# Kernel optimization log

Measured on AMD Instinct MI355X. Metric: run time of the kernel, lower is better.

## Reference

```python
import jax, jax.numpy as jnp
import numpy as np
import math

B, L, H, NH = 4, 2048, 256, 8
DH = H // NH

def setup_inputs() -> dict:
    key = jax.random.key(0)
    ks = jax.random.split(key, 10)
    q = jax.random.normal(ks[0], (B, L, H), dtype=jnp.float32)
    k = jax.random.normal(ks[1], (B, L, H), dtype=jnp.float32)
    v = jax.random.normal(ks[2], (B, L, H), dtype=jnp.float32)
    k_b = jax.random.normal(ks[3], (B, L, H), dtype=jnp.float32)
    mask = jnp.ones((B, L), dtype=jnp.int32)
    # learned params
    scale_w = jax.random.normal(ks[4], (NH, L), dtype=jnp.float32)
    Wb = jax.random.normal(ks[5], (H, H), dtype=jnp.float32) * (1.0 / math.sqrt(H))
    bb = jnp.zeros((H,), dtype=jnp.float32)
    Ww = jax.random.normal(ks[6], (H, H), dtype=jnp.float32) * (1.0 / math.sqrt(H))
    bw = jnp.zeros((H,), dtype=jnp.float32)
    return {"q": q, "k": k, "v": v, "k_b": k_b, "mask": mask,
            "scale_w": scale_w, "Wb": Wb, "bb": bb, "Ww": Ww, "bw": bw}

def _split_heads(x):
    b, l, _ = x.shape
    return x.reshape(b, l, NH, DH).transpose(0, 2, 1, 3)  # [B, NH, L, DH]

def reference(q, k, v, k_b, mask, scale_w, Wb, bb, Ww, bw):
    qh = _split_heads(q)
    kh = _split_heads(k)
    vh = _split_heads(v)
    kb = _split_heads(k_b @ Wb.T + bb)
    # dual QK^T: [B, NH, L, L]
    corr = jnp.einsum('bhqd,bhkd->bhqk', qh, kh) + jnp.einsum('bhqd,bhkd->bhqk', qh, kb)
    corr = corr * (1.0 / math.sqrt(DH))
    # per-head, per-query-position learned scale
    corr = corr * scale_w[None, :, :, None]
    # mask over key positions: [B,1,1,L]
    corr = jnp.where(mask[:, None, None, :] == 0, jnp.float32(-1e9), corr)
    prob = jax.nn.softmax(corr, axis=-1)
    hidden = jnp.einsum('bhqk,bhkd->bhqd', prob, vh)  # [B, NH, L, DH]
    hidden = hidden.transpose(0, 2, 1, 3).reshape(hidden.shape[0], -1, NH * DH)
    return hidden @ Ww.T + bw
```

## Files before the change

kernel.cpp:

```cpp
#include <hip/hip_runtime.h>
#include <stdint.h>
#include <stddef.h>


#define B_ 4
#define L_ 2048
#define H_ 256
#define NH_ 8
#define DH_ 32

typedef float    f32x4  __attribute__((ext_vector_type(4)));
typedef float    f32x16 __attribute__((ext_vector_type(16)));
typedef __bf16   bf16x8 __attribute__((ext_vector_type(8)));
typedef uint16_t u16x4  __attribute__((ext_vector_type(4)));
typedef uint16_t u16x8  __attribute__((ext_vector_type(8)));

static __device__ __forceinline__ uint16_t f2bf(float f) {
  __bf16 h = (__bf16)f;
  return __builtin_bit_cast(uint16_t, h);
}

static __device__ __forceinline__ void gl16(const void* g, void* l) {
  __builtin_amdgcn_global_load_lds(
      (const __attribute__((address_space(1))) uint32_t*)g,
      (__attribute__((address_space(3))) uint32_t*)l, 16, 0, 0);
}

#define OFF_KSUM 0
#define OFF_VTP  (OFF_KSUM + (size_t)B_*NH_*L_*DH_*2)
#define OFF_HID  (OFF_VTP  + (size_t)B_*NH_*L_*DH_*2)
#define OFF_FLAG (OFF_HID  + (size_t)B_*L_*H_*2)


__global__ __launch_bounds__(512, 1) void prep_k(const float* __restrict__ kb,
                                                 const float* __restrict__ wb,
                                                 const float* __restrict__ kin,
                                                 const float* __restrict__ bb,
                                                 const float* __restrict__ v,
                                                 const int* __restrict__ mask,
                                                 uint16_t* __restrict__ ksum_out,
                                                 uint16_t* __restrict__ vtp,
                                                 int* __restrict__ maskflag) {
  __shared__ uint16_t SM[65536];
  const int tid = threadIdx.x;

  if (blockIdx.x == 768) {
    if (tid < 4) maskflag[tid] = 0;
    __syncthreads();
    int b = tid >> 7, seg = tid & 127;
    int bad = 0;
#pragma unroll
    for (int i = 0; i < 16; i++) bad |= (mask[b * 2048 + seg * 16 + i] == 0);
    if (bad) atomicOr(&maskflag[b], 1);
    return;
  }

  if (blockIdx.x < 512) {
    uint16_t (*T)[33] = (uint16_t(*)[33])SM;
    const int bh = blockIdx.x >> 4, t = blockIdx.x & 15;
    const int b = bh >> 3, h = bh & 7;
    {
      int r = tid >> 2, qtr = tid & 3;
      const float* src = v + ((size_t)(b * 2048 + t * 128 + r)) * 256 + h * 32 + qtr * 8;
      f32x4 s0 = *(const f32x4*)(src);
      f32x4 s1 = *(const f32x4*)(src + 4);
#pragma unroll
      for (int i = 0; i < 4; i++) {
        T[r][qtr * 8 + i]     = f2bf(s0[i]);
        T[r][qtr * 8 + 4 + i] = f2bf(s1[i]);
      }
    }
    __syncthreads();
    {
      int slot = tid >> 5, d = tid & 31;
      int kg = slot >> 2, s = (slot >> 1) & 1, hii = slot & 1;
      u16x8 val;
#pragma unroll
      for (int e = 0; e < 8; e++) {
        int key = kg * 32 + s * 16 + 4 * hii + (e & 3) + 8 * (e >> 2);
        val[e] = T[key][d];
      }
      *(u16x8*)(vtp + (size_t)bh * 65536 + t * 4096 + slot * 256 + d * 8) = val;
    }
    return;
  }

  uint16_t* WB = SM;
  const int mblk = blockIdx.x - 512;
  const int wv = tid >> 6, lane = tid & 63;
  const int g = lane >> 4, qi = lane & 15;
  const int rt = wv & 1, ch = wv >> 1;
  const int m = mblk * 32 + rt * 16 + qi;
  const int n0 = ch * 64;

#pragma unroll
  for (int s = 0; s < 16; s++) {
    int gid = s * 512 + tid;
    int n = gid >> 5, gl = gid & 31;
    const float* src = wb + (size_t)n * 256 + gl * 8;
    f32x4 a0 = *(const f32x4*)src;
    f32x4 a1 = *(const f32x4*)(src + 4);
    u16x8 val;
#pragma unroll
    for (int i = 0; i < 4; i++) { val[i] = f2bf(a0[i]); val[4 + i] = f2bf(a1[i]); }
    *(u16x8*)&WB[n * 256 + (gl ^ (n & 7)) * 8] = val;
  }
  __syncthreads();

  f32x4 acc[4];
#pragma unroll
  for (int i = 0; i < 4; i++) acc[i] = (f32x4){0.f, 0.f, 0.f, 0.f};

#pragma unroll
  for (int ks = 0; ks < 8; ks++) {
    const float* ap = kb + (size_t)m * 256 + ks * 32 + g * 8;
    f32x4 a0 = *(const f32x4*)ap;
    f32x4 a1 = *(const f32x4*)(ap + 4);
    bf16x8 af;
#pragma unroll
    for (int i = 0; i < 4; i++) { af[i] = (__bf16)a0[i]; af[4 + i] = (__bf16)a1[i]; }
#pragma unroll
    for (int nt = 0; nt < 4; nt++) {
      int n = n0 + nt * 16 + qi;
      bf16x8 bf = *(const bf16x8*)&WB[n * 256 + ((ks * 4 + g) ^ (n & 7)) * 8];
      acc[nt] = __builtin_amdgcn_mfma_f32_16x16x32_bf16(af, bf, acc[nt], 0, 0, 0);
    }
  }
#pragma unroll
  for (int nt = 0; nt < 4; nt++) {
    int n = n0 + nt * 16 + qi;
    float bbv = bb[n];
    int h = n >> 5, d = n & 31;
#pragma unroll
    for (int j = 0; j < 4; j++) {
      int mr = mblk * 32 + rt * 16 + g * 4 + j;
      float val = acc[nt][j] + bbv + kin[(size_t)mr * 256 + n];
      int bq = mr >> 11, l = mr & 2047;
      size_t off = (size_t)(bq * 8 + h) * 65536 +
                   (l >> 5) * 1024 + (d >> 4) * 512 + (l & 31) * 16 + (d & 15);
      ksum_out[off] = f2bf(val);
    }
  }
}

__global__ __launch_bounds__(256, 2) void attn_k(const float* __restrict__ q,
                                                 const int* __restrict__ mask,
                                                 const float* __restrict__ scale_w,
                                                 const uint16_t* __restrict__ ksum,
                                                 const uint16_t* __restrict__ vtp,
                                                 const int* __restrict__ maskflag,
                                                 uint16_t* __restrict__ hid) {
  __shared__ __align__(16) uint16_t KV[2][8192];

  const int bid = blockIdx.x;
  const int bh = bid & 31, qblk = bid >> 5;
  const int b = bh >> 3, h = bh & 7;
  const int tid = threadIdx.x, wv = tid >> 6, lane = tid & 63;
  const int qi = lane & 31, hi = lane >> 5;
  const int qrow = qblk * 128 + wv * 32 + qi;

  const float scale = scale_w[h * 2048 + qrow] * (0.17677669529663687f * 1.4426950408889634f);
  const float* qp = q + ((size_t)(b * 2048 + qrow)) * 256 + h * 32;
  bf16x8 qf0, qf1;
  {
    f32x4 a0 = *(const f32x4*)(qp + hi * 8);
    f32x4 a1 = *(const f32x4*)(qp + hi * 8 + 4);
    f32x4 c0 = *(const f32x4*)(qp + 16 + hi * 8);
    f32x4 c1 = *(const f32x4*)(qp + 16 + hi * 8 + 4);
#pragma unroll
    for (int i = 0; i < 4; i++) {
      qf0[i] = (__bf16)(a0[i] * scale); qf0[4 + i] = (__bf16)(a1[i] * scale);
      qf1[i] = (__bf16)(c0[i] * scale); qf1[4 + i] = (__bf16)(c1[i] * scale);
    }
  }

  const uint16_t* kbase = ksum + (size_t)bh * 65536;
  const uint16_t* vbase = vtp + (size_t)bh * 65536;
  const bool allmask = (maskflag[b] == 0);

#define STAGE(tt, bufp)                                                                      \
  {                                                                                          \
    _Pragma("unroll")                                                                        \
    for (int i_ = 0; i_ < 2; i_++) {                                                         \
      gl16(kbase + (tt) * 4096 + (wv * 2 + i_) * 512 + lane * 8, (bufp) + (wv * 2 + i_) * 512); \
      gl16(vbase + (tt) * 4096 + (wv * 2 + i_) * 512 + lane * 8, (bufp) + 4096 + (wv * 2 + i_) * 512); \
    }                                                                                        \
  }
  STAGE(0, &KV[0][0]);
  STAGE(1, &KV[1][0]);

  float lsa[4] = {0.f, 0.f, 0.f, 0.f};
  f32x16 Oa, Ob, Z0;
#pragma unroll
  for (int i = 0; i < 16; i++) { Oa[i] = 0.f; Ob[i] = 0.f; Z0[i] = 0.f; }

  for (int t = 0; t < 16; t++) {
    uint16_t* bufp = &KV[t & 1][0];
    if (t < 15) { asm volatile("s_waitcnt vmcnt(4)" ::: "memory"); }
    else        { asm volatile("s_waitcnt vmcnt(0)" ::: "memory"); }
    __builtin_amdgcn_sched_barrier(0);
    __builtin_amdgcn_s_barrier();

    const uint16_t* Kl = bufp;
    const uint16_t* Vl = bufp + 4096;
#pragma unroll
    for (int kg = 0; kg < 4; kg++) {
      bf16x8 kf0 = *(const bf16x8*)&Kl[kg * 1024 + qi * 16 + hi * 8];
      bf16x8 kf1 = *(const bf16x8*)&Kl[kg * 1024 + 512 + qi * 16 + hi * 8];
      f32x16 S;
      __builtin_amdgcn_s_setprio(1);
      S = __builtin_amdgcn_mfma_f32_32x32x16_bf16(kf0, qf0, Z0, 0, 0, 0);
      S = __builtin_amdgcn_mfma_f32_32x32x16_bf16(kf1, qf1, S, 0, 0, 0);
      __builtin_amdgcn_s_setprio(0);

      if (!allmask) {
        const int* mrow = mask + b * 2048 + t * 128 + kg * 32 + 4 * hi;
#pragma unroll
        for (int r = 0; r < 16; r++)
          if (mrow[(r & 3) + 8 * (r >> 2)] == 0) S[r] = -1.0e9f;
      }

      bf16x8 pa0, pa1;
#pragma unroll
      for (int r = 0; r < 8; r++) {
        float p = __builtin_amdgcn_exp2f(S[r]);
        pa0[r] = (__bf16)p;
        lsa[r & 3] += p;
      }
#pragma unroll
      for (int r = 0; r < 8; r++) {
        float p = __builtin_amdgcn_exp2f(S[8 + r]);
        pa1[r] = (__bf16)p;
        lsa[r & 3] += p;
      }

      bf16x8 vf0 = *(const bf16x8*)&Vl[(kg * 4 + hi) * 256 + qi * 8];
      bf16x8 vf1 = *(const bf16x8*)&Vl[(kg * 4 + 2 + hi) * 256 + qi * 8];
      __builtin_amdgcn_s_setprio(1);
      Oa = __builtin_amdgcn_mfma_f32_32x32x16_bf16(vf0, pa0, Oa, 0, 0, 0);
      Ob = __builtin_amdgcn_mfma_f32_32x32x16_bf16(vf1, pa1, Ob, 0, 0, 0);
      __builtin_amdgcn_s_setprio(0);
    }

    __builtin_amdgcn_s_barrier();
    if (t < 14) STAGE(t + 2, bufp);
  }
#undef STAGE

  float l = (lsa[0] + lsa[1]) + (lsa[2] + lsa[3]);
  l += __shfl_xor(l, 32);
  const float inv = 1.0f / l;
  uint16_t* hp = hid + ((size_t)(b * 2048 + qrow)) * 256 + h * 32;
#pragma unroll
  for (int grp = 0; grp < 4; grp++) {
    u16x4 st;
#pragma unroll
    for (int j = 0; j < 4; j++) st[j] = f2bf((Oa[grp * 4 + j] + Ob[grp * 4 + j]) * inv);
    *(u16x4*)(hp + grp * 8 + hi * 4) = st;
  }
}

__global__ __launch_bounds__(512, 1) void oproj_k(const uint16_t* __restrict__ hid,
                                                  const float* __restrict__ ww,
                                                  const float* __restrict__ bw,
                                                  float* __restrict__ out) {
  __shared__ uint16_t WW[65536];
  const int tid = threadIdx.x;
  const int mblk = blockIdx.x;
  const int wv = tid >> 6, lane = tid & 63;
  const int g = lane >> 4, qi = lane & 15;
  const int rt = wv & 1, ch = wv >> 1;
  const int m = mblk * 32 + rt * 16 + qi;
  const int n0 = ch * 64;

#pragma unroll
  for (int s = 0; s < 16; s++) {
    int gid = s * 512 + tid;
    int n = gid >> 5, gl = gid & 31;
    const float* src = ww + (size_t)n * 256 + gl * 8;
    f32x4 a0 = *(const f32x4*)src;
    f32x4 a1 = *(const f32x4*)(src + 4);
    u16x8 val;
#pragma unroll
    for (int i = 0; i < 4; i++) { val[i] = f2bf(a0[i]); val[4 + i] = f2bf(a1[i]); }
    *(u16x8*)&WW[n * 256 + (gl ^ (n & 7)) * 8] = val;
  }
  __syncthreads();

  f32x4 acc[4];
#pragma unroll
  for (int i = 0; i < 4; i++) acc[i] = (f32x4){0.f, 0.f, 0.f, 0.f};

#pragma unroll
  for (int ks = 0; ks < 8; ks++) {
    bf16x8 af = *(const bf16x8*)(hid + (size_t)m * 256 + ks * 32 + g * 8);
#pragma unroll
    for (int nt = 0; nt < 4; nt++) {
      int n = n0 + nt * 16 + qi;
      bf16x8 bf = *(const bf16x8*)&WW[n * 256 + ((ks * 4 + g) ^ (n & 7)) * 8];
      acc[nt] = __builtin_amdgcn_mfma_f32_16x16x32_bf16(af, bf, acc[nt], 0, 0, 0);
    }
  }
#pragma unroll
  for (int nt = 0; nt < 4; nt++) {
    int n = n0 + nt * 16 + qi;
    float bwv = bw[n];
#pragma unroll
    for (int j = 0; j < 4; j++) {
      int mr = mblk * 32 + rt * 16 + g * 4 + j;
      out[(size_t)mr * 256 + n] = acc[nt][j] + bwv;
    }
  }
}

extern "C" void kernel_launch(void* const* d_in, const int* in_sizes, int n_in,
                              void* d_out, int out_size, void* d_ws, size_t ws_size,
                              hipStream_t stream) {
  const float* q       = (const float*)d_in[0];
  const float* k       = (const float*)d_in[1];
  const float* v       = (const float*)d_in[2];
  const float* kb      = (const float*)d_in[3];
  const int*   mask    = (const int*)d_in[4];
  const float* scale_w = (const float*)d_in[5];
  const float* Wb      = (const float*)d_in[6];
  const float* bb      = (const float*)d_in[7];
  const float* Ww      = (const float*)d_in[8];
  const float* bw      = (const float*)d_in[9];

  char* ws = (char*)d_ws;
  uint16_t* ksum  = (uint16_t*)(ws + OFF_KSUM);
  uint16_t* vtp   = (uint16_t*)(ws + OFF_VTP);
  uint16_t* hid   = (uint16_t*)(ws + OFF_HID);
  int* maskflag   = (int*)(ws + OFF_FLAG);
  float* out = (float*)d_out;

  prep_k<<<dim3(769), dim3(512), 0, stream>>>(kb, Wb, k, bb, v, mask, ksum, vtp, maskflag);
  attn_k<<<dim3(512), dim3(256), 0, stream>>>(q, mask, scale_w, ksum, vtp, maskflag, hid);
  oproj_k<<<dim3(256), dim3(512), 0, stream>>>(hid, Ww, bw, out);
}
```

Measured before the change: 50.35 us.

## Deepen attention K/V pipeline to four stages and precompute swizzled bf16 Ww

The attention kernel now keeps four K/V tiles in LDS instead of two. Each barrier interval processes two tiles and prefetches two more, which halves the number of barriers and keeps more loads in flight. Separately, the fp32-to-bf16 conversion and swizzle of Ww moves into extra blocks of the prep kernel. The output-projection kernel then fills LDS with direct global-to-LDS copies instead of having each of its 256 blocks redo the conversion. LDS per attention block doubles to 64KB, which may limit occupancy of the two-blocks-per-CU launch bound.

Measured after the change: 48.88 us, median of 2. 1.03x faster.

```diff
diff --git a/kernel.cpp b/kernel.cpp
--- a/kernel.cpp
+++ b/kernel.cpp
@@ -30,6 +30,7 @@
 #define OFF_VTP  (OFF_KSUM + (size_t)B_*NH_*L_*DH_*2)
 #define OFF_HID  (OFF_VTP  + (size_t)B_*NH_*L_*DH_*2)
 #define OFF_FLAG (OFF_HID  + (size_t)B_*L_*H_*2)
+#define OFF_WWF  (OFF_FLAG + 64)
 
 
 __global__ __launch_bounds__(512, 1) void prep_k(const float* __restrict__ kb,
@@ -38,11 +39,27 @@
                                                  const float* __restrict__ bb,
                                                  const float* __restrict__ v,
                                                  const int* __restrict__ mask,
+                                                 const float* __restrict__ ww,
                                                  uint16_t* __restrict__ ksum_out,
                                                  uint16_t* __restrict__ vtp,
-                                                 int* __restrict__ maskflag) {
+                                                 int* __restrict__ maskflag,
+                                                 uint16_t* __restrict__ wwf) {
   __shared__ uint16_t SM[65536];
   const int tid = threadIdx.x;
+
+  if (blockIdx.x >= 769) {
+    int gid = (blockIdx.x - 769) * 512 + tid;
+    int n = gid >> 5, gpos = gid & 31;
+    int gl = gpos ^ (n & 7);
+    const float* src = ww + (size_t)n * 256 + gl * 8;
+    f32x4 a0 = *(const f32x4*)src;
+    f32x4 a1 = *(const f32x4*)(src + 4);
+    u16x8 val;
+#pragma unroll
+    for (int i = 0; i < 4; i++) { val[i] = f2bf(a0[i]); val[4 + i] = f2bf(a1[i]); }
+    *(u16x8*)(wwf + (size_t)gid * 8) = val;
+    return;
+  }
 
   if (blockIdx.x == 768) {
     if (tid < 4) maskflag[tid] = 0;
@@ -150,7 +167,7 @@
                                                  const uint16_t* __restrict__ vtp,
                                                  const int* __restrict__ maskflag,
                                                  uint16_t* __restrict__ hid) {
-  __shared__ __align__(16) uint16_t KV[2][8192];
+  __shared__ __align__(16) uint16_t KV[4][8192];
 
   const int bid = blockIdx.x;
   const int bh = bid & 31, qblk = bid >> 5;
@@ -188,62 +205,70 @@
   }
   STAGE(0, &KV[0][0]);
   STAGE(1, &KV[1][0]);
+  STAGE(2, &KV[2][0]);
+  STAGE(3, &KV[3][0]);
 
   float lsa[4] = {0.f, 0.f, 0.f, 0.f};
   f32x16 Oa, Ob, Z0;
 #pragma unroll
   for (int i = 0; i < 16; i++) { Oa[i] = 0.f; Ob[i] = 0.f; Z0[i] = 0.f; }
 
-  for (int t = 0; t < 16; t++) {
-    uint16_t* bufp = &KV[t & 1][0];
-    if (t < 15) { asm volatile("s_waitcnt vmcnt(4)" ::: "memory"); }
-    else        { asm volatile("s_waitcnt vmcnt(0)" ::: "memory"); }
+  for (int p = 0; p < 8; p++) {
+    if (p < 7) { asm volatile("s_waitcnt vmcnt(8)" ::: "memory"); }
+    else       { asm volatile("s_waitcnt vmcnt(0)" ::: "memory"); }
     __builtin_amdgcn_sched_barrier(0);
     __builtin_amdgcn_s_barrier();
 
-    const uint16_t* Kl = bufp;
-    const uint16_t* Vl = bufp + 4096;
-#pragma unroll
-    for (int kg = 0; kg < 4; kg++) {
-      bf16x8 kf0 = *(const bf16x8*)&Kl[kg * 1024 + qi * 16 + hi * 8];
-      bf16x8 kf1 = *(const bf16x8*)&Kl[kg * 1024 + 512 + qi * 16 + hi * 8];
-      f32x16 S;
-      __builtin_amdgcn_s_setprio(1);
-      S = __builtin_amdgcn_mfma_f32_32x32x16_bf16(kf0, qf0, Z0, 0, 0, 0);
-      S = __builtin_amdgcn_mfma_f32_32x32x16_bf16(kf1, qf1, S, 0, 0, 0);
-      __builtin_amdgcn_s_setprio(0);
-
-      if (!allmask) {
-        const int* mrow = mask + b * 2048 + t * 128 + kg * 32 + 4 * hi;
-#pragma unroll
-        for (int r = 0; r < 16; r++)
-          if (mrow[(r & 3) + 8 * (r >> 2)] == 0) S[r] = -1.0e9f;
+#pragma unroll
+    for (int ti = 0; ti < 2; ti++) {
+      const int t = 2 * p + ti;
+      const uint16_t* Kl = &KV[t & 3][0];
+      const uint16_t* Vl = Kl + 4096;
+#pragma unroll
+      for (int kg = 0; kg < 4; kg++) {
+        bf16x8 kf0 = *(const bf16x8*)&Kl[kg * 1024 + qi * 16 + hi * 8];
+        bf16x8 kf1 = *(const bf16x8*)&Kl[kg * 1024 + 512 + qi * 16 + hi * 8];
+        f32x16 S;
+        __builtin_amdgcn_s_setprio(1);
+        S = __builtin_amdgcn_mfma_f32_32x32x16_bf16(kf0, qf0, Z0, 0, 0, 0);
+        S = __builtin_amdgcn_mfma_f32_32x32x16_bf16(kf1, qf1, S, 0, 0, 0);
+        __builtin_amdgcn_s_setprio(0);
+
+        if (!allmask) {
+          const int* mrow = mask + b * 2048 + t * 128 + kg * 32 + 4 * hi;
+#pragma unroll
+          for (int r = 0; r < 16; r++)
+            if (mrow[(r & 3) + 8 * (r >> 2)] == 0) S[r] = -1.0e9f;
+        }
+
+        bf16x8 pa0, pa1;
+#pragma unroll
+        for (int r = 0; r < 8; r++) {
+          float pv = __builtin_amdgcn_exp2f(S[r]);
+          pa0[r] = (__bf16)pv;
+          lsa[r & 3] += pv;
+        }
+#pragma unroll
+        for (int r = 0; r < 8; r++) {
+          float pv = __builtin_amdgcn_exp2f(S[8 + r]);
+          pa1[r] = (__bf16)pv;
+          lsa[r & 3] += pv;
+        }
+
+        bf16x8 vf0 = *(const bf16x8*)&Vl[(kg * 4 + hi) * 256 + qi * 8];
+        bf16x8 vf1 = *(const bf16x8*)&Vl[(kg * 4 + 2 + hi) * 256 + qi * 8];
+        __builtin_amdgcn_s_setprio(1);
+        Oa = __builtin_amdgcn_mfma_f32_32x32x16_bf16(vf0, pa0, Oa, 0, 0, 0);
+        Ob = __builtin_amdgcn_mfma_f32_32x32x16_bf16(vf1, pa1, Ob, 0, 0, 0);
+        __builtin_amdgcn_s_setprio(0);
       }
-
-      bf16x8 pa0, pa1;
-#pragma unroll
-      for (int r = 0; r < 8; r++) {
-        float p = __builtin_amdgcn_exp2f(S[r]);
-        pa0[r] = (__bf16)p;
-        lsa[r & 3] += p;
-      }
-#pragma unroll
-      for (int r = 0; r < 8; r++) {
-        float p = __builtin_amdgcn_exp2f(S[8 + r]);
-        pa1[r] = (__bf16)p;
-        lsa[r & 3] += p;
-      }
-
-      bf16x8 vf0 = *(const bf16x8*)&Vl[(kg * 4 + hi) * 256 + qi * 8];
-      bf16x8 vf1 = *(const bf16x8*)&Vl[(kg * 4 + 2 + hi) * 256 + qi * 8];
-      __builtin_amdgcn_s_setprio(1);
-      Oa = __builtin_amdgcn_mfma_f32_32x32x16_bf16(vf0, pa0, Oa, 0, 0, 0);
-      Ob = __builtin_amdgcn_mfma_f32_32x32x16_bf16(vf1, pa1, Ob, 0, 0, 0);
-      __builtin_amdgcn_s_setprio(0);
     }
 
     __builtin_amdgcn_s_barrier();
-    if (t < 14) STAGE(t + 2, bufp);
+    if (p < 6) {
+      STAGE(2 * p + 4, &KV[(2 * p) & 3][0]);
+      STAGE(2 * p + 5, &KV[(2 * p + 1) & 3][0]);
+    }
   }
 #undef STAGE
 
@@ -261,10 +286,10 @@
 }
 
 __global__ __launch_bounds__(512, 1) void oproj_k(const uint16_t* __restrict__ hid,
-                                                  const float* __restrict__ ww,
+                                                  const uint16_t* __restrict__ wwf,
                                                   const float* __restrict__ bw,
                                                   float* __restrict__ out) {
-  __shared__ uint16_t WW[65536];
+  __shared__ __align__(16) uint16_t WW[65536];
   const int tid = threadIdx.x;
   const int mblk = blockIdx.x;
   const int wv = tid >> 6, lane = tid & 63;
@@ -274,17 +299,8 @@
   const int n0 = ch * 64;
 
 #pragma unroll
-  for (int s = 0; s < 16; s++) {
-    int gid = s * 512 + tid;
-    int n = gid >> 5, gl = gid & 31;
-    const float* src = ww + (size_t)n * 256 + gl * 8;
-    f32x4 a0 = *(const f32x4*)src;
-    f32x4 a1 = *(const f32x4*)(src + 4);
-    u16x8 val;
-#pragma unroll
-    for (int i = 0; i < 4; i++) { val[i] = f2bf(a0[i]); val[4 + i] = f2bf(a1[i]); }
-    *(u16x8*)&WW[n * 256 + (gl ^ (n & 7)) * 8] = val;
-  }
+  for (int i = 0; i < 16; i++)
+    gl16(wwf + (size_t)(i * 512 + wv * 64 + lane) * 8, &WW[(i * 512 + wv * 64) * 8]);
   __syncthreads();
 
   f32x4 acc[4];
@@ -332,9 +348,10 @@
   uint16_t* vtp   = (uint16_t*)(ws + OFF_VTP);
   uint16_t* hid   = (uint16_t*)(ws + OFF_HID);
   int* maskflag   = (int*)(ws + OFF_FLAG);
+  uint16_t* wwf   = (uint16_t*)(ws + OFF_WWF);
   float* out = (float*)d_out;
 
-  prep_k<<<dim3(769), dim3(512), 0, stream>>>(kb, Wb, k, bb, v, mask, ksum, vtp, maskflag);
+  prep_k<<<dim3(785), dim3(512), 0, stream>>>(kb, Wb, k, bb, v, mask, Ww, ksum, vtp, maskflag, wwf);
   attn_k<<<dim3(512), dim3(256), 0, stream>>>(q, mask, scale_w, ksum, vtp, maskflag, hid);
-  oproj_k<<<dim3(256), dim3(512), 0, stream>>>(hid, Ww, bw, out);
-}
+  oproj_k<<<dim3(256), dim3(512), 0, stream>>>(hid, wwf, bw, out);
+}
```
